# Kernel optimization log

Measured on AMD Instinct MI355X. Metric: run time of the kernel, lower is better.

Reference implementation:

```python
import jax, jax.numpy as jnp
import numpy as np

B, R, CIN, J, O, ITERS = 512, 1152, 8, 10, 16, 3  # batch, routes, in_ch, capsules, out_ch, routing iters


def squash(s, axis):
    # v = (||s||^2 / (1 + ||s||^2)) * s / ||s||  (standard CapsNet squash)
    sq = jnp.sum(s * s, axis=axis, keepdims=True)
    return (sq / (1.0 + sq)) * s * jax.lax.rsqrt(sq + 1e-8)


def setup_inputs() -> dict:
    key = jax.random.key(0)
    k1, k2 = jax.random.split(key)
    x = jax.random.normal(k1, (B, R, CIN), dtype=jnp.float32)
    W = jax.random.normal(k2, (R, J, O, CIN), dtype=jnp.float32)  # param, batch-broadcast
    return {"x": x, "W": W}


def reference(x, W):
    # u_hat[b,r,j,:] = W[r,j] @ x[b,r]   (replaces torch stack/cat broadcasting)
    u_hat = jnp.einsum('rjoc,brc->brjo', W, x)  # [B,R,J,O]
    b_ij = jnp.zeros((x.shape[0], R, J), dtype=x.dtype)
    v = None
    for it in range(ITERS):
        c_ij = jax.nn.softmax(b_ij, axis=2)                 # softmax over capsules j
        s_j = jnp.einsum('brj,brjo->bjo', c_ij, u_hat)      # weighted sum over routes
        v = squash(s_j, axis=-1)                            # [B,J,O]
        if it < ITERS - 1:
            b_ij = b_ij + jnp.einsum('brjo,bjo->brj', u_hat, v)  # agreement
    # torch returns v_j.squeeze(1) with shape [B, J, O, 1]
    return v[..., None]
```

## Files before the change

kernel.cpp:

```cpp
#include <hip/hip_runtime.h>
#include <hip/hip_fp16.h>
#include <cstdint>
#include <cstddef>

#define NB 512
#define NR 1152
#define NC 8
#define NJ 10
#define NO 16
#define NJO 160

typedef unsigned int uint32;

union H2U { __half2 h; uint32 u; };

__device__ __forceinline__ uint32 packf16(float a0, float a1) {
    H2U p;
    p.h = __halves2half2(__float2half_rn(a0), __float2half_rn(a1));
    return p.u;
}
__device__ __forceinline__ float2 unpackf16(uint32 w) {
    H2U p; p.u = w;
    return __half22float2(p.h);
}

__global__ __launch_bounds__(256) void xpose_kernel(const float* __restrict__ x,
                                                    float* __restrict__ xT) {
    const int r0 = blockIdx.x * 16;
    const int b0 = blockIdx.y * 64;
    const int t  = threadIdx.x;
    __shared__ float tile[16][65][8];

    for (int i = t; i < 2048; i += 256) {
        int b = i >> 5, r = (i >> 1) & 15, h = i & 1;
        float4 v = *(const float4*)&x[(size_t)(b0 + b) * (NR * NC) + (size_t)(r0 + r) * NC + h * 4];
        *(float4*)&tile[r][b][h * 4] = v;
    }
    __syncthreads();
    for (int i = t; i < 2048; i += 256) {
        int r = i >> 7, b = (i >> 1) & 63, h = i & 1;
        float4 v = *(const float4*)&tile[r][b][h * 4];
        *(float4*)&xT[(size_t)(r0 + r) * (NB * NC) + (size_t)(b0 + b) * NC + h * 4] = v;
    }
}

__global__ __launch_bounds__(320) void uhat_kernel(const float* __restrict__ xT,
                                                   const float* __restrict__ W,
                                                   uint32* __restrict__ u) {
    const int r = blockIdx.x;
    const int t = threadIdx.x;

    __shared__ float Ws[NC][NJO + 4];
    __shared__ float xs[NB][NC];

    for (int i = t; i < NJO * NC; i += 320) {
        Ws[i & 7][i >> 3] = W[(size_t)r * (NJO * NC) + i];
    }
    {
        const float4* xsrc = (const float4*)(xT + (size_t)r * (NB * NC));
        float4* xdst = (float4*)&xs[0][0];
        for (int i = t; i < (NB * NC) / 4; i += 320) xdst[i] = xsrc[i];
    }
    __syncthreads();

    const int ni   = t % 80;
    const int half = t / 80;
    const int qt  = ni / 20;
    const int rem = ni % 20;
    const int j   = rem >> 1;
    const int d   = rem & 1;
    const int jo0 = 16 * j + 4 * qt + 2 * d;

    float w0[8], w1[8];
#pragma unroll
    for (int c = 0; c < 8; ++c) {
        w0[c] = Ws[c][jo0];
        w1[c] = Ws[c][jo0 + 1];
    }

    for (int b = half; b < NB; b += 4) {
        const float4* xp = (const float4*)xs[b];
        float4 xa = xp[0], xb = xp[1];
        float a0 = w0[0] * xa.x + w0[1] * xa.y + w0[2] * xa.z + w0[3] * xa.w
                 + w0[4] * xb.x + w0[5] * xb.y + w0[6] * xb.z + w0[7] * xb.w;
        float a1 = w1[0] * xa.x + w1[1] * xa.y + w1[2] * xa.z + w1[3] * xa.w
                 + w1[4] * xb.x + w1[5] * xb.y + w1[6] * xb.z + w1[7] * xb.w;
        u[(size_t)(b * NR + r) * 80 + ni] = packf16(a0, a1);
    }
}

__global__ __launch_bounds__(576, 2) void routing_kernel(const uint32* __restrict__ u,
                                                         float* __restrict__ outp) {
    const int b  = blockIdx.x;
    const int t  = threadIdx.x;
    const int w  = t >> 6;
    const int l  = t & 63;
    const int m  = (l >> 2) & 15;
    const int qt = l & 3;

    __shared__ float sl[NJO];
    __shared__ float vls[NJO];
    __shared__ float vaccl[NJO];

    for (int i = t; i < NJO; i += 576) sl[i] = 0.0f;
    __syncthreads();

    const uint32* ubase = u + (size_t)b * (NR * 80) + qt * 20;

#pragma unroll 1
    for (int it = 0; it < 3; ++it) {
        float acc[40];
#pragma unroll
        for (int i = 0; i < 40; ++i) acc[i] = 0.0f;

#pragma unroll 1
        for (int c8 = 0; c8 < 8; ++c8) {
            const int r = (w * 8 + c8) * 16 + m;
            const uint4* up = (const uint4*)(ubase + (size_t)r * 80);
            uint32 ur[20];
#pragma unroll
            for (int i = 0; i < 5; ++i) {
                uint4 q = up[i];
                ur[4 * i + 0] = q.x; ur[4 * i + 1] = q.y;
                ur[4 * i + 2] = q.z; ur[4 * i + 3] = q.w;
            }

            float cj[NJ];
            if (it == 0) {
#pragma unroll
                for (int j = 0; j < NJ; ++j) cj[j] = 0.1f;
            } else {
                float sum = 0.0f;
#pragma unroll
                for (int j = 0; j < NJ; ++j) {
                    float2 ua = unpackf16(ur[2 * j]);
                    float2 ub = unpackf16(ur[2 * j + 1]);
                    float4 vv = *(const float4*)&vls[16 * j + 4 * qt];
                    float pj = ua.x * vv.x + ua.y * vv.y + ub.x * vv.z + ub.y * vv.w;
                    pj += __shfl_xor(pj, 1);
                    pj += __shfl_xor(pj, 2);
                    float e = __expf(pj);
                    cj[j] = e;
                    sum += e;
                }
                float inv = 1.0f / sum;
#pragma unroll
                for (int j = 0; j < NJ; ++j) cj[j] *= inv;
            }

#pragma unroll
            for (int j = 0; j < NJ; ++j) {
                float2 ua = unpackf16(ur[2 * j]);
                float2 ub = unpackf16(ur[2 * j + 1]);
                acc[4 * j + 0] += cj[j] * ua.x;
                acc[4 * j + 1] += cj[j] * ua.y;
                acc[4 * j + 2] += cj[j] * ub.x;
                acc[4 * j + 3] += cj[j] * ub.y;
            }
        }

        float a[24];
        {
            const int bit = (l >> 2) & 1;
#pragma unroll
            for (int i = 0; i < 24; ++i) {
                float lo = acc[i];
                float hi = (i + 24 < 40) ? acc[i + 24] : 0.0f;
                float send = bit ? lo : hi;
                float recv = __shfl_xor(send, 4);
                a[i] = (bit ? hi : lo) + recv;
            }
        }
#pragma unroll
        for (int st = 1; st < 4; ++st) {
            const int h = 24 >> st;
            const int bit = (l >> (2 + st)) & 1;
#pragma unroll
            for (int i = 0; i < 12; ++i) {
                if (i < h) {
                    float send = bit ? a[i] : a[i + h];
                    float recv = __shfl_xor(send, 4 << st);
                    a[i] = (bit ? a[i + h] : a[i]) + recv;
                }
            }
        }
        const int base = 3 * (__brev((uint32)m) >> 28);
#pragma unroll
        for (int i = 0; i < 3; ++i) {
            int aidx = base + i;
            if (aidx < 40) {
                int j = aidx >> 2, e = aidx & 3;
                atomicAdd(&sl[16 * j + 4 * qt + e], a[i]);
            }
        }
        __syncthreads();

        if (t < 80) {
            float2 sv = *(const float2*)&sl[2 * t];
            float sq = sv.x * sv.x + sv.y * sv.y;
#pragma unroll
            for (int off = 1; off < 8; off <<= 1) sq += __shfl_xor(sq, off, 8);
            float scale = (sq / (1.0f + sq)) * rsqrtf(sq + 1e-8f);
            float vx = sv.x * scale, vy = sv.y * scale;
            if (it == 2) {
                *(float2*)&outp[b * NJO + 2 * t] = make_float2(vx, vy);
            } else {
                float2 va;
                if (it == 0) va = make_float2(vx, vy);
                else {
                    va = *(const float2*)&vaccl[2 * t];
                    va.x += vx; va.y += vy;
                }
                *(float2*)&vaccl[2 * t] = va;
                *(float2*)&vls[2 * t]   = va;
            }
        }
        __syncthreads();
        if (it < 2) {
            for (int i = t; i < NJO; i += 576) sl[i] = 0.0f;
            __syncthreads();
        }
    }
}

extern "C" void kernel_launch(void* const* d_in, const int* in_sizes, int n_in,
                              void* d_out, int out_size, void* d_ws, size_t ws_size,
                              hipStream_t stream) {
    (void)in_sizes; (void)n_in; (void)out_size; (void)ws_size;

    const float* x = (const float*)d_in[0];
    const float* W = (const float*)d_in[1];
    float* out = (float*)d_out;

    char* ws = (char*)d_ws;
    const size_t XBYTES = (size_t)NR * NB * NC * 4;
    float*  xT = (float*)ws;
    uint32* u  = (uint32*)(ws + XBYTES);

    xpose_kernel<<<dim3(NR / 16, NB / 64), 256, 0, stream>>>(x, xT);
    uhat_kernel<<<NR, 320, 0, stream>>>(xT, W, u);
    routing_kernel<<<NB, 576, 0, stream>>>(u, out);
}
```

Measured before the change: 219.4 us.

## Fuse first routing iteration's weighted sum into u_hat kernel via partial sums

The u_hat kernel now tiles over 64 routes by 32 batches and accumulates the uniform-coefficient sum of u_hat per batch while it produces it. It writes 18 partial sums per batch to workspace. The routing kernel reduces these partials to get the first iteration's s_j and starts at iteration 1, which removes one full pass over the u_hat tensor. The cost is fewer u_hat blocks (18x16), more synchronisation per route, extra partial buffer traffic, and first-iteration sums computed in fp32 before fp16 rounding.

```diff
diff --git a/kernel.cpp b/kernel.cpp
--- a/kernel.cpp
+++ b/kernel.cpp
@@ -9,6 +9,7 @@
 #define NJ 10
 #define NO 16
 #define NJO 160
+#define KSP 18
 
 typedef unsigned int uint32;
 
@@ -44,52 +45,68 @@
     }
 }
 
-__global__ __launch_bounds__(320) void uhat_kernel(const float* __restrict__ xT,
-                                                   const float* __restrict__ W,
-                                                   uint32* __restrict__ u) {
-    const int r = blockIdx.x;
-    const int t = threadIdx.x;
-
-    __shared__ float Ws[NC][NJO + 4];
-    __shared__ float xs[NB][NC];
-
-    for (int i = t; i < NJO * NC; i += 320) {
-        Ws[i & 7][i >> 3] = W[(size_t)r * (NJO * NC) + i];
-    }
-    {
-        const float4* xsrc = (const float4*)(xT + (size_t)r * (NB * NC));
-        float4* xdst = (float4*)&xs[0][0];
-        for (int i = t; i < (NB * NC) / 4; i += 320) xdst[i] = xsrc[i];
-    }
-    __syncthreads();
-
-    const int ni   = t % 80;
-    const int half = t / 80;
+__global__ __launch_bounds__(320) void uhat_s0_kernel(const float* __restrict__ xT,
+                                                      const float* __restrict__ W,
+                                                      uint32* __restrict__ u,
+                                                      float* __restrict__ part) {
+    const int r0 = blockIdx.x * 64;
+    const int b0 = blockIdx.y * 32;
+    const int t  = threadIdx.x;
+
+    const int ni = t % 80;
+    const int bg = t / 80;
     const int qt  = ni / 20;
     const int rem = ni % 20;
     const int j   = rem >> 1;
     const int d   = rem & 1;
     const int jo0 = 16 * j + 4 * qt + 2 * d;
 
-    float w0[8], w1[8];
-#pragma unroll
-    for (int c = 0; c < 8; ++c) {
-        w0[c] = Ws[c][jo0];
-        w1[c] = Ws[c][jo0 + 1];
-    }
-
-    for (int b = half; b < NB; b += 4) {
-        const float4* xp = (const float4*)xs[b];
-        float4 xa = xp[0], xb = xp[1];
-        float a0 = w0[0] * xa.x + w0[1] * xa.y + w0[2] * xa.z + w0[3] * xa.w
-                 + w0[4] * xb.x + w0[5] * xb.y + w0[6] * xb.z + w0[7] * xb.w;
-        float a1 = w1[0] * xa.x + w1[1] * xa.y + w1[2] * xa.z + w1[3] * xa.w
-                 + w1[4] * xb.x + w1[5] * xb.y + w1[6] * xb.z + w1[7] * xb.w;
-        u[(size_t)(b * NR + r) * 80 + ni] = packf16(a0, a1);
+    __shared__ float xs[32][8];
+
+    float sacc[8][2];
+#pragma unroll
+    for (int k = 0; k < 8; ++k) { sacc[k][0] = 0.0f; sacc[k][1] = 0.0f; }
+
+#pragma unroll 1
+    for (int rr = 0; rr < 64; ++rr) {
+        const int r = r0 + rr;
+        __syncthreads();
+        if (t < 64) {
+            int bb = t >> 1, h = t & 1;
+            *(float4*)&xs[bb][h * 4] =
+                *(const float4*)&xT[(size_t)r * (NB * NC) + (b0 + bb) * 8 + h * 4];
+        }
+        __syncthreads();
+
+        const float4* wp = (const float4*)&W[(size_t)r * (NJO * NC) + jo0 * 8];
+        float4 w0a = wp[0], w0b = wp[1], w1a = wp[2], w1b = wp[3];
+
+#pragma unroll
+        for (int k = 0; k < 8; ++k) {
+            const int bl = bg + 4 * k;
+            const float4* xp = (const float4*)xs[bl];
+            float4 xa = xp[0], xb = xp[1];
+            float a0 = w0a.x * xa.x + w0a.y * xa.y + w0a.z * xa.z + w0a.w * xa.w
+                     + w0b.x * xb.x + w0b.y * xb.y + w0b.z * xb.z + w0b.w * xb.w;
+            float a1 = w1a.x * xa.x + w1a.y * xa.y + w1a.z * xa.z + w1a.w * xa.w
+                     + w1b.x * xb.x + w1b.y * xb.y + w1b.z * xb.z + w1b.w * xb.w;
+            u[((size_t)(b0 + bl) * NR + r) * 80 + ni] = packf16(a0, a1);
+            sacc[k][0] += a0;
+            sacc[k][1] += a1;
+        }
+    }
+
+    float* pb = part + (size_t)blockIdx.x * (NB * NJO);
+#pragma unroll
+    for (int k = 0; k < 8; ++k) {
+        float* pp = pb + (size_t)(b0 + bg + 4 * k) * NJO + jo0;
+        pp[0] = sacc[k][0];
+        pp[1] = sacc[k][1];
     }
 }
 
 __global__ __launch_bounds__(576, 2) void routing_kernel(const uint32* __restrict__ u,
+                                                         const float* __restrict__ part,
                                                          float* __restrict__ outp) {
     const int b  = blockIdx.x;
     const int t  = threadIdx.x;
@@ -102,13 +119,33 @@
     __shared__ float vls[NJO];
     __shared__ float vaccl[NJO];
 
-    for (int i = t; i < NJO; i += 576) sl[i] = 0.0f;
+    if (t < NJO) {
+        float s = 0.0f;
+#pragma unroll
+        for (int k = 0; k < KSP; ++k) s += part[(size_t)k * (NB * NJO) + b * NJO + t];
+        sl[t] = 0.1f * s;
+    }
     __syncthreads();
 
+    if (t < 80) {
+        float2 sv = *(const float2*)&sl[2 * t];
+        float sq = sv.x * sv.x + sv.y * sv.y;
+#pragma unroll
+        for (int off = 1; off < 8; off <<= 1) sq += __shfl_xor(sq, off, 8);
+        float scale = (sq / (1.0f + sq)) * rsqrtf(sq + 1e-8f);
+        float2 va = make_float2(sv.x * scale, sv.y * scale);
+        *(float2*)&vaccl[2 * t] = va;
+        *(float2*)&vls[2 * t]   = va;
+    }
+    __syncthreads();
+
     const uint32* ubase = u + (size_t)b * (NR * 80) + qt * 20;
 
 #pragma unroll 1
-    for (int it = 0; it < 3; ++it) {
+    for (int it = 1; it < 3; ++it) {
+        for (int i = t; i < NJO; i += 576) sl[i] = 0.0f;
+        __syncthreads();
+
         float acc[40];
 #pragma unroll
         for (int i = 0; i < 40; ++i) acc[i] = 0.0f;
@@ -126,10 +163,7 @@
             }
 
             float cj[NJ];
-            if (it == 0) {
-#pragma unroll
-                for (int j = 0; j < NJ; ++j) cj[j] = 0.1f;
-            } else {
+            {
                 float sum = 0.0f;
 #pragma unroll
                 for (int j = 0; j < NJ; ++j) {
@@ -205,21 +239,13 @@
             if (it == 2) {
                 *(float2*)&outp[b * NJO + 2 * t] = make_float2(vx, vy);
             } else {
-                float2 va;
-                if (it == 0) va = make_float2(vx, vy);
-                else {
-                    va = *(const float2*)&vaccl[2 * t];
-                    va.x += vx; va.y += vy;
-                }
+                float2 va = *(const float2*)&vaccl[2 * t];
+                va.x += vx; va.y += vy;
                 *(float2*)&vaccl[2 * t] = va;
                 *(float2*)&vls[2 * t]   = va;
             }
         }
         __syncthreads();
-        if (it < 2) {
-            for (int i = t; i < NJO; i += 576) sl[i] = 0.0f;
-            __syncthreads();
-        }
     }
 }
 
@@ -234,10 +260,12 @@
 
     char* ws = (char*)d_ws;
     const size_t XBYTES = (size_t)NR * NB * NC * 4;
-    float*  xT = (float*)ws;
-    uint32* u  = (uint32*)(ws + XBYTES);
+    const size_t UBYTES = (size_t)NB * NR * 80 * 4;
+    float*  xT   = (float*)ws;
+    uint32* u    = (uint32*)(ws + XBYTES);
+    float*  part = (float*)(ws + XBYTES + UBYTES);
 
     xpose_kernel<<<dim3(NR / 16, NB / 64), 256, 0, stream>>>(x, xT);
-    uhat_kernel<<<NR, 320, 0, stream>>>(xT, W, u);
-    routing_kernel<<<NB, 576, 0, stream>>>(u, out);
-}
+    uhat_s0_kernel<<<dim3(KSP, NB / 32), 320, 0, stream>>>(xT, W, u, part);
+    routing_kernel<<<NB, 576, 0, stream>>>(u, part, out);
+}
```

Result: slower. 261.3 us (+19.1%).
